# Kernel tuning notes

Measured on AMD Instinct MI355X. Metric: run time of the kernel, lower is better.

## Reference

```python
import jax, jax.numpy as jnp
import numpy as np

N_NODES = 50000


def gcn_conv(x, W, b, src, dst, n_nodes):
    # PyG GCNConv: add self-loops, symmetric normalization, linear, scatter-add.
    loop = jnp.arange(n_nodes, dtype=src.dtype)
    s = jnp.concatenate([src, loop])  # [E+N]
    d = jnp.concatenate([dst, loop])
    deg = jax.ops.segment_sum(jnp.ones_like(d, dtype=x.dtype), d, num_segments=n_nodes)
    dinv = jnp.where(deg > 0, deg ** -0.5, 0.0)
    norm = dinv[s] * dinv[d]  # [E+N]
    h = x @ W  # [N, F_out] transform first (cheaper than per-edge)
    msg = h[s] * norm[:, None]  # gather + scale
    out = jax.ops.segment_sum(msg, d, num_segments=n_nodes)  # scatter-add
    return out + b


def setup_inputs() -> dict:
    key = jax.random.key(0)
    k1, k2, k3, k4, k5 = jax.random.split(key, 5)
    n_in, n_hid, n_out = 128, 128, 64
    x = jax.random.normal(k1, (N_NODES, n_in), dtype=jnp.float32)
    edge_index = jax.random.randint(k2, (2, 800000), 0, N_NODES, dtype=jnp.int64)
    edge_label_index = jax.random.randint(k3, (2, 200000), 0, N_NODES, dtype=jnp.int64)
    # Glorot-style init for GCN weights, zero bias (PyG default)
    W1 = jax.random.normal(k4, (n_in, n_hid), dtype=jnp.float32) * (1.0 / np.sqrt(n_in))
    W2 = jax.random.normal(k5, (n_hid, n_out), dtype=jnp.float32) * (1.0 / np.sqrt(n_hid))
    b1 = jnp.zeros((n_hid,), dtype=jnp.float32)
    b2 = jnp.zeros((n_out,), dtype=jnp.float32)
    return {"x": x, "edge_index": edge_index, "edge_label_index": edge_label_index,
            "W1": W1, "b1": b1, "W2": W2, "b2": b2}


def reference(x, edge_index, edge_label_index, W1, b1, W2, b2):
    src, dst = edge_index[0], edge_index[1]
    h = jax.nn.relu(gcn_conv(x, W1, b1, src, dst, N_NODES))
    z = gcn_conv(h, W2, b2, src, dst, N_NODES)
    # decode: per-edge dot product of endpoint embeddings
    logits = jnp.sum(z[edge_label_index[0]] * z[edge_label_index[1]], axis=-1)
    return logits
```

## Files before the change

kernel.cpp:

```cpp
#include <hip/hip_runtime.h>

#define N_NODES 50000
#define NB ((N_NODES + 255) / 256)


#define OFF_ROWPTR 50048
#define OFF_BSUM   100096
#define OFF_BOFF   100352
#define OFF_CNT    100608
#define OFF_ESRC   150656
#define OFF_EPOS   950656
#define OFF_H1B    1750784
#define OFF_OUT1   4950784
#define OFF_OUT2   11350784

__device__ __forceinline__ ushort f2bf(float f) {
  uint u = __float_as_uint(f);
  u += 0x7fffu + ((u >> 16) & 1u);
  return (ushort)(u >> 16);
}
__device__ __forceinline__ uint pack2(float a, float b) {
  return (uint)f2bf(a) | ((uint)f2bf(b) << 16);
}
__device__ __forceinline__ float blo(uint u) { return __uint_as_float(u << 16); }
__device__ __forceinline__ float bhi(uint u) { return __uint_as_float(u & 0xffff0000u); }

__global__ __launch_bounds__(256) void k_zero(int* __restrict__ cnt) {
  int i = blockIdx.x * 256 + threadIdx.x;
  if (i < N_NODES) cnt[i] = 0;
}

__global__ __launch_bounds__(256) void k_hist(const int* __restrict__ dst, int E,
                                              int* __restrict__ cnt,
                                              int* __restrict__ epos) {
  int i = blockIdx.x * 256 + threadIdx.x;
  if (i < E) epos[i] = atomicAdd(&cnt[dst[i]], 1);
}

__global__ __launch_bounds__(256) void k_scan1(const int* __restrict__ cnt,
                                               int* __restrict__ rowptr,
                                               int* __restrict__ bsum) {
  __shared__ int tmp[256];
  int i = blockIdx.x * 256 + threadIdx.x;
  int v = (i < N_NODES) ? cnt[i] : 0;
  tmp[threadIdx.x] = v;
  __syncthreads();
  for (int off = 1; off < 256; off <<= 1) {
    int t = (threadIdx.x >= off) ? tmp[threadIdx.x - off] : 0;
    __syncthreads();
    tmp[threadIdx.x] += t;
    __syncthreads();
  }
  if (i < N_NODES) rowptr[i] = tmp[threadIdx.x] - v;
  if (threadIdx.x == 255) bsum[blockIdx.x] = tmp[255];
}

__global__ __launch_bounds__(256) void k_scan2(const int* __restrict__ bsum,
                                               int* __restrict__ boff) {
  __shared__ int tmp[256];
  int v = (threadIdx.x < NB) ? bsum[threadIdx.x] : 0;
  tmp[threadIdx.x] = v;
  __syncthreads();
  for (int off = 1; off < 256; off <<= 1) {
    int t = (threadIdx.x >= off) ? tmp[threadIdx.x - off] : 0;
    __syncthreads();
    tmp[threadIdx.x] += t;
    __syncthreads();
  }
  if (threadIdx.x < NB) boff[threadIdx.x] = tmp[threadIdx.x] - v;
}

__global__ __launch_bounds__(256) void k_scan3(int* __restrict__ rowptr,
                                               const int* __restrict__ cnt,
                                               float* __restrict__ dinv,
                                               const int* __restrict__ boff, int E) {
  int i = blockIdx.x * 256 + threadIdx.x;
  if (i < N_NODES) {
    rowptr[i] += boff[blockIdx.x];
    dinv[i] = rsqrtf(1.0f + (float)cnt[i]);
  }
  if (i == 0) rowptr[N_NODES] = E;
}

__global__ __launch_bounds__(256) void k_fill(const int* __restrict__ src,
                                              const int* __restrict__ dst,
                                              const int* __restrict__ epos, int E,
                                              const int* __restrict__ rowptr,
                                              int* __restrict__ esrc) {
  int e = blockIdx.x * 256 + threadIdx.x;
  if (e < E) esrc[rowptr[dst[e]] + epos[e]] = src[e];
}

__global__ __launch_bounds__(256) void k_gemm1(const float* __restrict__ x,
                                               const float* __restrict__ W1,
                                               const float* __restrict__ dinv,
                                               ushort* __restrict__ h1b) {
  __shared__ float Wl[64 * 128];
  __shared__ float xs[64 * 68];
  const int tid = threadIdx.x;
  const int lane = tid & 63;
  const int wv = tid >> 6;
  const int cg = lane & 15;
  const int ng = wv * 4 + (lane >> 4);
  const int n0 = blockIdx.x * 64;
  const int c0 = cg * 4;

  float acc[4][8];
#pragma unroll
  for (int j = 0; j < 4; ++j)
#pragma unroll
    for (int c = 0; c < 8; ++c) acc[j][c] = 0.f;

  for (int kt = 0; kt < 2; ++kt) {
    for (int i = tid; i < 64 * 16; i += 256) {
      int nn = i >> 4, kq = i & 15;
      int gr = min(n0 + nn, N_NODES - 1);
      *(float4*)&xs[nn * 68 + kq * 4] =
          *(const float4*)&x[(size_t)gr * 128 + kt * 64 + kq * 4];
    }
    for (int i = tid; i < 64 * 32; i += 256) {
      int kk = i >> 5, cq = i & 31;
      *(float4*)&Wl[kk * 128 + cq * 4] =
          *(const float4*)&W1[(size_t)(kt * 64 + kk) * 128 + cq * 4];
    }
    __syncthreads();

    for (int k4 = 0; k4 < 64; k4 += 4) {
      float4 xa[4];
#pragma unroll
      for (int j = 0; j < 4; ++j)
        xa[j] = *(const float4*)&xs[(ng * 4 + j) * 68 + k4];
#pragma unroll
      for (int i = 0; i < 4; ++i) {
        float4 w0 = *(const float4*)&Wl[(k4 + i) * 128 + c0];
        float4 w1 = *(const float4*)&Wl[(k4 + i) * 128 + 64 + c0];
#pragma unroll
        for (int j = 0; j < 4; ++j) {
          float xv = i == 0 ? xa[j].x : i == 1 ? xa[j].y : i == 2 ? xa[j].z : xa[j].w;
          acc[j][0] = fmaf(xv, w0.x, acc[j][0]);
          acc[j][1] = fmaf(xv, w0.y, acc[j][1]);
          acc[j][2] = fmaf(xv, w0.z, acc[j][2]);
          acc[j][3] = fmaf(xv, w0.w, acc[j][3]);
          acc[j][4] = fmaf(xv, w1.x, acc[j][4]);
          acc[j][5] = fmaf(xv, w1.y, acc[j][5]);
          acc[j][6] = fmaf(xv, w1.z, acc[j][6]);
          acc[j][7] = fmaf(xv, w1.w, acc[j][7]);
        }
      }
    }
    __syncthreads();
  }

#pragma unroll
  for (int j = 0; j < 4; ++j) {
    int n = n0 + ng * 4 + j;
    if (n >= N_NODES) continue;
    float dl = dinv[n];
    uint2 p0, p1;
    p0.x = pack2(acc[j][0] * dl, acc[j][1] * dl);
    p0.y = pack2(acc[j][2] * dl, acc[j][3] * dl);
    p1.x = pack2(acc[j][4] * dl, acc[j][5] * dl);
    p1.y = pack2(acc[j][6] * dl, acc[j][7] * dl);
    *(uint2*)&h1b[(size_t)n * 128 + c0]      = p0;
    *(uint2*)&h1b[(size_t)n * 128 + 64 + c0] = p1;
  }
}

__global__ __launch_bounds__(256) void k_pull1(const int* __restrict__ rowptr,
                                               const int* __restrict__ esrc,
                                               const float* __restrict__ dinv,
                                               const uint* __restrict__ h1b,
                                               const float* __restrict__ b1,
                                               float* __restrict__ out1) {
  int n = (blockIdx.x * 256 + threadIdx.x) >> 6;
  int lane = threadIdx.x & 63;
  if (n >= N_NODES) return;
  int b = rowptr[n], e = rowptr[n + 1];
  int deg = e - b;

  uint u = h1b[(size_t)n * 64 + lane];
  float a0 = blo(u), a1 = bhi(u);

  int sidx = (lane < deg) ? esrc[b + lane] : 0;
  int kmax = deg < 64 ? deg : 64;
  int k = 0;
  for (; k + 7 < kmax; k += 8) {
    int s0 = __shfl(sidx, k + 0, 64), s1 = __shfl(sidx, k + 1, 64);
    int s2 = __shfl(sidx, k + 2, 64), s3 = __shfl(sidx, k + 3, 64);
    int s4 = __shfl(sidx, k + 4, 64), s5 = __shfl(sidx, k + 5, 64);
    int s6 = __shfl(sidx, k + 6, 64), s7 = __shfl(sidx, k + 7, 64);
    uint u0 = h1b[(size_t)s0 * 64 + lane];
    uint u1 = h1b[(size_t)s1 * 64 + lane];
    uint u2 = h1b[(size_t)s2 * 64 + lane];
    uint u3 = h1b[(size_t)s3 * 64 + lane];
    uint u4 = h1b[(size_t)s4 * 64 + lane];
    uint u5 = h1b[(size_t)s5 * 64 + lane];
    uint u6 = h1b[(size_t)s6 * 64 + lane];
    uint u7 = h1b[(size_t)s7 * 64 + lane];
    a0 += blo(u0) + blo(u1) + blo(u2) + blo(u3) + blo(u4) + blo(u5) + blo(u6) + blo(u7);
    a1 += bhi(u0) + bhi(u1) + bhi(u2) + bhi(u3) + bhi(u4) + bhi(u5) + bhi(u6) + bhi(u7);
  }
  for (; k < kmax; ++k) {
    int s = __shfl(sidx, k, 64);
    uint uu = h1b[(size_t)s * 64 + lane];
    a0 += blo(uu);
    a1 += bhi(uu);
  }
  for (int j = b + 64; j < e; ++j) {
    uint uu = h1b[(size_t)esrc[j] * 64 + lane];
    a0 += blo(uu);
    a1 += bhi(uu);
  }

  float dd = dinv[n];
  float2 bb = ((const float2*)b1)[lane];
  float2 o;
  o.x = fmaf(dd, a0, bb.x);
  o.y = fmaf(dd, a1, bb.y);
  ((float2*)out1)[(size_t)n * 64 + lane] = o;
}

__global__ __launch_bounds__(256) void k_gemm2(const float* __restrict__ out1,
                                               const float* __restrict__ W2,
                                               const float* __restrict__ dinv,
                                               ushort* __restrict__ h2b) {
  __shared__ float Wl[64 * 64];
  __shared__ float xs[64 * 68];
  const int tid = threadIdx.x;
  const int lane = tid & 63;
  const int wv = tid >> 6;
  const int cg = lane & 15;
  const int ng = wv * 4 + (lane >> 4);
  const int n0 = blockIdx.x * 64;
  const int c0 = cg * 4;

  float acc[4][4];
#pragma unroll
  for (int j = 0; j < 4; ++j)
#pragma unroll
    for (int c = 0; c < 4; ++c) acc[j][c] = 0.f;

  for (int kt = 0; kt < 2; ++kt) {
    for (int i = tid; i < 64 * 16; i += 256) {
      int nn = i >> 4, kq = i & 15;
      int gr = min(n0 + nn, N_NODES - 1);
      float4 v = *(const float4*)&out1[(size_t)gr * 128 + kt * 64 + kq * 4];
      v.x = fmaxf(v.x, 0.f); v.y = fmaxf(v.y, 0.f);
      v.z = fmaxf(v.z, 0.f); v.w = fmaxf(v.w, 0.f);
      *(float4*)&xs[nn * 68 + kq * 4] = v;
    }
    for (int i = tid; i < 64 * 16; i += 256) {
      int kk = i >> 4, cq = i & 15;
      *(float4*)&Wl[kk * 64 + cq * 4] =
          *(const float4*)&W2[(size_t)(kt * 64 + kk) * 64 + cq * 4];
    }
    __syncthreads();

    for (int k4 = 0; k4 < 64; k4 += 4) {
      float4 xa[4];
#pragma unroll
      for (int j = 0; j < 4; ++j)
        xa[j] = *(const float4*)&xs[(ng * 4 + j) * 68 + k4];
#pragma unroll
      for (int i = 0; i < 4; ++i) {
        float4 w0 = *(const float4*)&Wl[(k4 + i) * 64 + c0];
#pragma unroll
        for (int j = 0; j < 4; ++j) {
          float xv = i == 0 ? xa[j].x : i == 1 ? xa[j].y : i == 2 ? xa[j].z : xa[j].w;
          acc[j][0] = fmaf(xv, w0.x, acc[j][0]);
          acc[j][1] = fmaf(xv, w0.y, acc[j][1]);
          acc[j][2] = fmaf(xv, w0.z, acc[j][2]);
          acc[j][3] = fmaf(xv, w0.w, acc[j][3]);
        }
      }
    }
    __syncthreads();
  }

#pragma unroll
  for (int j = 0; j < 4; ++j) {
    int n = n0 + ng * 4 + j;
    if (n >= N_NODES) continue;
    float dl = dinv[n];
    uint2 p;
    p.x = pack2(acc[j][0] * dl, acc[j][1] * dl);
    p.y = pack2(acc[j][2] * dl, acc[j][3] * dl);
    *(uint2*)&h2b[(size_t)n * 64 + c0] = p;
  }
}

__global__ __launch_bounds__(256) void k_pull2(const int* __restrict__ rowptr,
                                               const int* __restrict__ esrc,
                                               const float* __restrict__ dinv,
                                               const ushort* __restrict__ h2b,
                                               const float* __restrict__ b2,
                                               float* __restrict__ out2) {
  int n = (blockIdx.x * 256 + threadIdx.x) >> 6;
  int lane = threadIdx.x & 63;
  if (n >= N_NODES) return;
  int b = rowptr[n], e = rowptr[n + 1];
  int deg = e - b;

  float a = __uint_as_float((uint)h2b[(size_t)n * 64 + lane] << 16);

  int sidx = (lane < deg) ? esrc[b + lane] : 0;
  int kmax = deg < 64 ? deg : 64;
  int k = 0;
  for (; k + 7 < kmax; k += 8) {
    int s0 = __shfl(sidx, k + 0, 64), s1 = __shfl(sidx, k + 1, 64);
    int s2 = __shfl(sidx, k + 2, 64), s3 = __shfl(sidx, k + 3, 64);
    int s4 = __shfl(sidx, k + 4, 64), s5 = __shfl(sidx, k + 5, 64);
    int s6 = __shfl(sidx, k + 6, 64), s7 = __shfl(sidx, k + 7, 64);
    ushort v0 = h2b[(size_t)s0 * 64 + lane];
    ushort v1 = h2b[(size_t)s1 * 64 + lane];
    ushort v2 = h2b[(size_t)s2 * 64 + lane];
    ushort v3 = h2b[(size_t)s3 * 64 + lane];
    ushort v4 = h2b[(size_t)s4 * 64 + lane];
    ushort v5 = h2b[(size_t)s5 * 64 + lane];
    ushort v6 = h2b[(size_t)s6 * 64 + lane];
    ushort v7 = h2b[(size_t)s7 * 64 + lane];
    a += __uint_as_float((uint)v0 << 16) + __uint_as_float((uint)v1 << 16)
       + __uint_as_float((uint)v2 << 16) + __uint_as_float((uint)v3 << 16)
       + __uint_as_float((uint)v4 << 16) + __uint_as_float((uint)v5 << 16)
       + __uint_as_float((uint)v6 << 16) + __uint_as_float((uint)v7 << 16);
  }
  for (; k < kmax; ++k) {
    int s = __shfl(sidx, k, 64);
    a += __uint_as_float((uint)h2b[(size_t)s * 64 + lane] << 16);
  }
  for (int j = b + 64; j < e; ++j)
    a += __uint_as_float((uint)h2b[(size_t)esrc[j] * 64 + lane] << 16);

  out2[(size_t)n * 64 + lane] = fmaf(dinv[n], a, b2[lane]);
}

__global__ __launch_bounds__(256) void k_decode(const int* __restrict__ ia,
                                                const int* __restrict__ ib,
                                                const float* __restrict__ z,
                                                float* __restrict__ out, int M) {
  const int sub = threadIdx.x & 15;
  int e = (blockIdx.x * 256 + threadIdx.x) >> 4;
  if (e >= M) return;
  int a = ia[e], b = ib[e];
  float4 va = ((const float4*)z)[(size_t)a * 16 + sub];
  float4 vb = ((const float4*)z)[(size_t)b * 16 + sub];
  float v = va.x * vb.x + va.y * vb.y + va.z * vb.z + va.w * vb.w;
  v += __shfl_xor(v, 8, 64);
  v += __shfl_xor(v, 4, 64);
  v += __shfl_xor(v, 2, 64);
  v += __shfl_xor(v, 1, 64);
  if (sub == 0) out[e] = v;
}

extern "C" void kernel_launch(void* const* d_in, const int* in_sizes, int n_in,
                              void* d_out, int out_size, void* d_ws, size_t ws_size,
                              hipStream_t stream) {
  const float* x   = (const float*)d_in[0];
  const int*   ei  = (const int*)d_in[1];
  const int*   eli = (const int*)d_in[2];
  const float* W1  = (const float*)d_in[3];
  const float* b1  = (const float*)d_in[4];
  const float* W2  = (const float*)d_in[5];
  const float* b2  = (const float*)d_in[6];
  float* outp = (float*)d_out;

  const int E = in_sizes[1] / 2;
  const int M = in_sizes[2] / 2;
  const int* src = ei;
  const int* dst = ei + E;
  const int* la  = eli;
  const int* lb  = eli + M;

  float* ws     = (float*)d_ws;
  float* dinv   = ws;
  int*   rowptr = (int*)(ws + OFF_ROWPTR);
  int*   bsum   = (int*)(ws + OFF_BSUM);
  int*   boff   = (int*)(ws + OFF_BOFF);
  int*   cnt    = (int*)(ws + OFF_CNT);
  int*   esrc   = (int*)(ws + OFF_ESRC);
  int*   epos   = (int*)(ws + OFF_EPOS);
  ushort* h1b   = (ushort*)(ws + OFF_H1B);
  ushort* h2b   = (ushort*)(ws + OFF_H1B);
  float* out1   = ws + OFF_OUT1;
  float* out2   = ws + OFF_OUT2;

  k_zero <<<NB, 256, 0, stream>>>(cnt);
  k_hist <<<(E + 255) / 256, 256, 0, stream>>>(dst, E, cnt, epos);
  k_scan1<<<NB, 256, 0, stream>>>(cnt, rowptr, bsum);
  k_scan2<<<1, 256, 0, stream>>>(bsum, boff);
  k_scan3<<<NB, 256, 0, stream>>>(rowptr, cnt, dinv, boff, E);
  k_fill <<<(E + 255) / 256, 256, 0, stream>>>(src, dst, epos, E, rowptr, esrc);

  k_gemm1<<<(N_NODES + 63) / 64, 256, 0, stream>>>(x, W1, dinv, h1b);
  k_pull1<<<12500, 256, 0, stream>>>(rowptr, esrc, dinv, (const uint*)h1b, b1, out1);

  k_gemm2<<<(N_NODES + 63) / 64, 256, 0, stream>>>(out1, W2, dinv, h2b);
  k_pull2<<<12500, 256, 0, stream>>>(rowptr, esrc, dinv, h2b, b2, out2);

  k_decode<<<12500, 256, 0, stream>>>(la, lb, out2, outp, M);
}
```

Baseline: 262.2 us.

## Use fp16 MFMA for both GCN dense transforms with pre-transposed swizzled weights

Replaces the scalar FP32 FMA GEMMs for the two linear layers with MFMA 16x16x32 fp16 instructions. A new prep kernel converts W1 and W2 to fp16, transposes them and applies an XOR swizzle. Activation tiles are converted to fp16 and stored swizzled in shared memory to avoid bank conflicts. This trades some input precision (fp16 operands, fp32 accumulate) for matrix-core throughput, though the GEMMs are a small part of a gather-dominated pipeline.

```diff
diff --git a/kernel.cpp b/kernel.cpp
--- a/kernel.cpp
+++ b/kernel.cpp
@@ -2,6 +2,10 @@
 
 #define N_NODES 50000
 #define NB ((N_NODES + 255) / 256)
+
+using half8 = __attribute__((ext_vector_type(8))) _Float16;
+using half4 = __attribute__((ext_vector_type(4))) _Float16;
+using f32x4 = __attribute__((ext_vector_type(4))) float;
 
 
 #define OFF_ROWPTR 50048
@@ -10,9 +14,11 @@
 #define OFF_CNT    100608
 #define OFF_ESRC   150656
 #define OFF_EPOS   950656
-#define OFF_H1B    1750784
-#define OFF_OUT1   4950784
-#define OFF_OUT2   11350784
+#define OFF_W1T    1750656
+#define OFF_W2T    1758848
+#define OFF_H1B    1762944
+#define OFF_OUT1   4962944
+#define OFF_OUT2   11362944
 
 __device__ __forceinline__ ushort f2bf(float f) {
   uint u = __float_as_uint(f);
@@ -91,78 +97,76 @@
   if (e < E) esrc[rowptr[dst[e]] + epos[e]] = src[e];
 }
 
+__global__ __launch_bounds__(256) void k_prep(const float* __restrict__ W1,
+                                              const float* __restrict__ W2,
+                                              _Float16* __restrict__ W1t,
+                                              _Float16* __restrict__ W2t) {
+  int i = blockIdx.x * 256 + threadIdx.x;
+  if (i < 16384) {
+    int c = i >> 7, k = i & 127;
+    W1t[c * 128 + (k ^ ((c & 7) << 3))] = (_Float16)W1[k * 128 + c];
+  } else if (i < 24576) {
+    int j = i - 16384;
+    int c = j >> 7, k = j & 127;
+    W2t[c * 128 + (k ^ ((c & 7) << 3))] = (_Float16)W2[k * 64 + c];
+  }
+}
+
 __global__ __launch_bounds__(256) void k_gemm1(const float* __restrict__ x,
-                                               const float* __restrict__ W1,
+                                               const _Float16* __restrict__ W1t,
                                                const float* __restrict__ dinv,
                                                ushort* __restrict__ h1b) {
-  __shared__ float Wl[64 * 128];
-  __shared__ float xs[64 * 68];
+  __shared__ _Float16 Wl[128 * 128];
+  __shared__ _Float16 xs[64 * 128];
   const int tid = threadIdx.x;
   const int lane = tid & 63;
   const int wv = tid >> 6;
-  const int cg = lane & 15;
-  const int ng = wv * 4 + (lane >> 4);
   const int n0 = blockIdx.x * 64;
-  const int c0 = cg * 4;
-
-  float acc[4][8];
-#pragma unroll
-  for (int j = 0; j < 4; ++j)
-#pragma unroll
-    for (int c = 0; c < 8; ++c) acc[j][c] = 0.f;
-
-  for (int kt = 0; kt < 2; ++kt) {
-    for (int i = tid; i < 64 * 16; i += 256) {
-      int nn = i >> 4, kq = i & 15;
-      int gr = min(n0 + nn, N_NODES - 1);
-      *(float4*)&xs[nn * 68 + kq * 4] =
-          *(const float4*)&x[(size_t)gr * 128 + kt * 64 + kq * 4];
+
+  for (int i = tid; i < 128 * 128 / 8; i += 256)
+    *(float4*)&Wl[i * 8] = *(const float4*)&W1t[i * 8];
+  for (int i = tid; i < 64 * 32; i += 256) {
+    int nn = i >> 5, k4 = (i & 31) * 4;
+    int gr = min(n0 + nn, N_NODES - 1);
+    float4 v = *(const float4*)&x[(size_t)gr * 128 + k4];
+    half4 hv;
+    hv[0] = (_Float16)v.x; hv[1] = (_Float16)v.y;
+    hv[2] = (_Float16)v.z; hv[3] = (_Float16)v.w;
+    *(half4*)&xs[nn * 128 + (k4 ^ ((nn & 7) << 3))] = hv;
+  }
+  __syncthreads();
+
+  f32x4 acc[8];
+#pragma unroll
+  for (int c = 0; c < 8; ++c) acc[c] = (f32x4){0.f, 0.f, 0.f, 0.f};
+
+  const int m15 = lane & 15;
+  const int kc = lane >> 4;
+  const int xrow = wv * 16 + m15;
+
+#pragma unroll
+  for (int kt = 0; kt < 4; ++kt) {
+    int e0 = kt * 32 + kc * 8;
+    half8 bfrag = *(half8*)&xs[xrow * 128 + (e0 ^ ((xrow & 7) << 3))];
+#pragma unroll
+    for (int ct = 0; ct < 8; ++ct) {
+      int wrow = ct * 16 + m15;
+      half8 afrag = *(half8*)&Wl[wrow * 128 + (e0 ^ ((wrow & 7) << 3))];
+      acc[ct] = __builtin_amdgcn_mfma_f32_16x16x32_f16(afrag, bfrag, acc[ct], 0, 0, 0);
     }
-    for (int i = tid; i < 64 * 32; i += 256) {
-      int kk = i >> 5, cq = i & 31;
-      *(float4*)&Wl[kk * 128 + cq * 4] =
-          *(const float4*)&W1[(size_t)(kt * 64 + kk) * 128 + cq * 4];
+  }
+
+  int n = n0 + wv * 16 + m15;
+  if (n < N_NODES) {
+    float dl = dinv[n];
+#pragma unroll
+    for (int ct = 0; ct < 8; ++ct) {
+      int c = ct * 16 + kc * 4;
+      uint2 p;
+      p.x = pack2(acc[ct][0] * dl, acc[ct][1] * dl);
+      p.y = pack2(acc[ct][2] * dl, acc[ct][3] * dl);
+      *(uint2*)&h1b[(size_t)n * 128 + c] = p;
     }
-    __syncthreads();
-
-    for (int k4 = 0; k4 < 64; k4 += 4) {
-      float4 xa[4];
-#pragma unroll
-      for (int j = 0; j < 4; ++j)
-        xa[j] = *(const float4*)&xs[(ng * 4 + j) * 68 + k4];
-#pragma unroll
-      for (int i = 0; i < 4; ++i) {
-        float4 w0 = *(const float4*)&Wl[(k4 + i) * 128 + c0];
-        float4 w1 = *(const float4*)&Wl[(k4 + i) * 128 + 64 + c0];
-#pragma unroll
-        for (int j = 0; j < 4; ++j) {
-          float xv = i == 0 ? xa[j].x : i == 1 ? xa[j].y : i == 2 ? xa[j].z : xa[j].w;
-          acc[j][0] = fmaf(xv, w0.x, acc[j][0]);
-          acc[j][1] = fmaf(xv, w0.y, acc[j][1]);
-          acc[j][2] = fmaf(xv, w0.z, acc[j][2]);
-          acc[j][3] = fmaf(xv, w0.w, acc[j][3]);
-          acc[j][4] = fmaf(xv, w1.x, acc[j][4]);
-          acc[j][5] = fmaf(xv, w1.y, acc[j][5]);
-          acc[j][6] = fmaf(xv, w1.z, acc[j][6]);
-          acc[j][7] = fmaf(xv, w1.w, acc[j][7]);
-        }
-      }
-    }
-    __syncthreads();
-  }
-
-#pragma unroll
-  for (int j = 0; j < 4; ++j) {
-    int n = n0 + ng * 4 + j;
-    if (n >= N_NODES) continue;
-    float dl = dinv[n];
-    uint2 p0, p1;
-    p0.x = pack2(acc[j][0] * dl, acc[j][1] * dl);
-    p0.y = pack2(acc[j][2] * dl, acc[j][3] * dl);
-    p1.x = pack2(acc[j][4] * dl, acc[j][5] * dl);
-    p1.y = pack2(acc[j][6] * dl, acc[j][7] * dl);
-    *(uint2*)&h1b[(size_t)n * 128 + c0]      = p0;
-    *(uint2*)&h1b[(size_t)n * 128 + 64 + c0] = p1;
   }
 }
 
@@ -221,71 +225,60 @@
 }
 
 __global__ __launch_bounds__(256) void k_gemm2(const float* __restrict__ out1,
-                                               const float* __restrict__ W2,
+                                               const _Float16* __restrict__ W2t,
                                                const float* __restrict__ dinv,
                                                ushort* __restrict__ h2b) {
-  __shared__ float Wl[64 * 64];
-  __shared__ float xs[64 * 68];
+  __shared__ _Float16 Wl[64 * 128];
+  __shared__ _Float16 xs[64 * 128];
   const int tid = threadIdx.x;
   const int lane = tid & 63;
   const int wv = tid >> 6;
-  const int cg = lane & 15;
-  const int ng = wv * 4 + (lane >> 4);
   const int n0 = blockIdx.x * 64;
-  const int c0 = cg * 4;
-
-  float acc[4][4];
-#pragma unroll
-  for (int j = 0; j < 4; ++j)
-#pragma unroll
-    for (int c = 0; c < 4; ++c) acc[j][c] = 0.f;
-
-  for (int kt = 0; kt < 2; ++kt) {
-    for (int i = tid; i < 64 * 16; i += 256) {
-      int nn = i >> 4, kq = i & 15;
-      int gr = min(n0 + nn, N_NODES - 1);
-      float4 v = *(const float4*)&out1[(size_t)gr * 128 + kt * 64 + kq * 4];
-      v.x = fmaxf(v.x, 0.f); v.y = fmaxf(v.y, 0.f);
-      v.z = fmaxf(v.z, 0.f); v.w = fmaxf(v.w, 0.f);
-      *(float4*)&xs[nn * 68 + kq * 4] = v;
+
+  for (int i = tid; i < 64 * 128 / 8; i += 256)
+    *(float4*)&Wl[i * 8] = *(const float4*)&W2t[i * 8];
+  for (int i = tid; i < 64 * 32; i += 256) {
+    int nn = i >> 5, k4 = (i & 31) * 4;
+    int gr = min(n0 + nn, N_NODES - 1);
+    float4 v = *(const float4*)&out1[(size_t)gr * 128 + k4];
+    half4 hv;
+    hv[0] = (_Float16)fmaxf(v.x, 0.f); hv[1] = (_Float16)fmaxf(v.y, 0.f);
+    hv[2] = (_Float16)fmaxf(v.z, 0.f); hv[3] = (_Float16)fmaxf(v.w, 0.f);
+    *(half4*)&xs[nn * 128 + (k4 ^ ((nn & 7) << 3))] = hv;
+  }
+  __syncthreads();
+
+  f32x4 acc[4];
+#pragma unroll
+  for (int c = 0; c < 4; ++c) acc[c] = (f32x4){0.f, 0.f, 0.f, 0.f};
+
+  const int m15 = lane & 15;
+  const int kc = lane >> 4;
+  const int xrow = wv * 16 + m15;
+
+#pragma unroll
+  for (int kt = 0; kt < 4; ++kt) {
+    int e0 = kt * 32 + kc * 8;
+    half8 bfrag = *(half8*)&xs[xrow * 128 + (e0 ^ ((xrow & 7) << 3))];
+#pragma unroll
+    for (int ct = 0; ct < 4; ++ct) {
+      int wrow = ct * 16 + m15;
+      half8 afrag = *(half8*)&Wl[wrow * 128 + (e0 ^ ((wrow & 7) << 3))];
+      acc[ct] = __builtin_amdgcn_mfma_f32_16x16x32_f16(afrag, bfrag, acc[ct], 0, 0, 0);
     }
-    for (int i = tid; i < 64 * 16; i += 256) {
-      int kk = i >> 4, cq = i & 15;
-      *(float4*)&Wl[kk * 64 + cq * 4] =
-          *(const float4*)&W2[(size_t)(kt * 64 + kk) * 64 + cq * 4];
+  }
+
+  int n = n0 + wv * 16 + m15;
+  if (n < N_NODES) {
+    float dl = dinv[n];
+#pragma unroll
+    for (int ct = 0; ct < 4; ++ct) {
+      int c = ct * 16 + kc * 4;
+      uint2 p;
+      p.x = pack2(acc[ct][0] * dl, acc[ct][1] * dl);
+      p.y = pack2(acc[ct][2] * dl, acc[ct][3] * dl);
+      *(uint2*)&h2b[(size_t)n * 64 + c] = p;
     }
-    __syncthreads();
-
-    for (int k4 = 0; k4 < 64; k4 += 4) {
-      float4 xa[4];
-#pragma unroll
-      for (int j = 0; j < 4; ++j)
-        xa[j] = *(const float4*)&xs[(ng * 4 + j) * 68 + k4];
-#pragma unroll
-      for (int i = 0; i < 4; ++i) {
-        float4 w0 = *(const float4*)&Wl[(k4 + i) * 64 + c0];
-#pragma unroll
-        for (int j = 0; j < 4; ++j) {
-          float xv = i == 0 ? xa[j].x : i == 1 ? xa[j].y : i == 2 ? xa[j].z : xa[j].w;
-          acc[j][0] = fmaf(xv, w0.x, acc[j][0]);
-          acc[j][1] = fmaf(xv, w0.y, acc[j][1]);
-          acc[j][2] = fmaf(xv, w0.z, acc[j][2]);
-          acc[j][3] = fmaf(xv, w0.w, acc[j][3]);
-        }
-      }
-    }
-    __syncthreads();
-  }
-
-#pragma unroll
-  for (int j = 0; j < 4; ++j) {
-    int n = n0 + ng * 4 + j;
-    if (n >= N_NODES) continue;
-    float dl = dinv[n];
-    uint2 p;
-    p.x = pack2(acc[j][0] * dl, acc[j][1] * dl);
-    p.y = pack2(acc[j][2] * dl, acc[j][3] * dl);
-    *(uint2*)&h2b[(size_t)n * 64 + c0] = p;
   }
 }
 
@@ -379,6 +372,8 @@
   int*   cnt    = (int*)(ws + OFF_CNT);
   int*   esrc   = (int*)(ws + OFF_ESRC);
   int*   epos   = (int*)(ws + OFF_EPOS);
+  _Float16* W1t = (_Float16*)(ws + OFF_W1T);
+  _Float16* W2t = (_Float16*)(ws + OFF_W2T);
   ushort* h1b   = (ushort*)(ws + OFF_H1B);
   ushort* h2b   = (ushort*)(ws + OFF_H1B);
   float* out1   = ws + OFF_OUT1;
@@ -386,15 +381,16 @@
 
   k_zero <<<NB, 256, 0, stream>>>(cnt);
   k_hist <<<(E + 255) / 256, 256, 0, stream>>>(dst, E, cnt, epos);
+  k_prep <<<96, 256, 0, stream>>>(W1, W2, W1t, W2t);
   k_scan1<<<NB, 256, 0, stream>>>(cnt, rowptr, bsum);
   k_scan2<<<1, 256, 0, stream>>>(bsum, boff);
   k_scan3<<<NB, 256, 0, stream>>>(rowptr, cnt, dinv, boff, E);
   k_fill <<<(E + 255) / 256, 256, 0, stream>>>(src, dst, epos, E, rowptr, esrc);
 
-  k_gemm1<<<(N_NODES + 63) / 64, 256, 0, stream>>>(x, W1, dinv, h1b);
+  k_gemm1<<<(N_NODES + 63) / 64, 256, 0, stream>>>(x, W1t, dinv, h1b);
   k_pull1<<<12500, 256, 0, stream>>>(rowptr, esrc, dinv, (const uint*)h1b, b1, out1);
 
-  k_gemm2<<<(N_NODES + 63) / 64, 256, 0, stream>>>(out1, W2, dinv, h2b);
+  k_gemm2<<<(N_NODES + 63) / 64, 256, 0, stream>>>(out1, W2t, dinv, h2b);
   k_pull2<<<12500, 256, 0, stream>>>(rowptr, esrc, dinv, h2b, b2, out2);
 
   k_decode<<<12500, 256, 0, stream>>>(la, lb, out2, outp, M);
```

Result: faster. 234.7 us (-10.5%).
